# Optimization experiments

Measured on AMD Instinct MI355X. Metric: run time of the kernel, lower is better.

The kernel has to match this reference:

```python
import jax, jax.numpy as jnp
import numpy as np

N_NODES = 100000
N_EDGES = 1600000
IN_FEATS = 128
H_FEATS = 64
NEG_SLOPE = 0.2


def gat_layer(x, W, a_l, a_r, b, src, dst):
    # x: [N, Fin], W: [Fin, Fout], a_l/a_r/b: [Fout]
    h = x @ W                                   # [N, Fout]
    el = h @ a_l                                # [N]
    er = h @ a_r                                # [N]
    e = el[src] + er[dst]                       # [E]
    e = jnp.where(e > 0, e, NEG_SLOPE * e)      # leaky_relu
    # segment softmax over incoming edges of each dst node
    m = jax.ops.segment_max(e, dst, num_segments=N_NODES)   # [N], -inf for deg-0
    ex = jnp.exp(e - m[dst])                                 # [E]
    s = jax.ops.segment_sum(ex, dst, num_segments=N_NODES)   # [N]
    alpha = ex / s[dst]                                      # [E]
    out = jax.ops.segment_sum(alpha[:, None] * h[src], dst, num_segments=N_NODES)
    return jax.nn.relu(out + b)


def setup_inputs() -> dict:
    key = jax.random.key(0)
    ks = jax.random.split(key, 16)
    in_feat = jax.random.normal(ks[0], (N_NODES, IN_FEATS), dtype=jnp.float32)
    src = jax.random.randint(ks[1], (N_EDGES,), 0, N_NODES, dtype=jnp.int32)
    dst = jax.random.randint(ks[2], (N_EDGES,), 0, N_NODES, dtype=jnp.int32)
    def w(k, fin, fout):
        return jax.random.normal(k, (fin, fout), dtype=jnp.float32) * (1.0 / np.sqrt(fin))
    def v(k, f):
        return jax.random.normal(k, (f,), dtype=jnp.float32) * 0.1
    return {
        "in_feat": in_feat, "src": src, "dst": dst,
        "W1": w(ks[3], IN_FEATS, H_FEATS), "al1": v(ks[4], H_FEATS), "ar1": v(ks[5], H_FEATS), "b1": jnp.zeros((H_FEATS,), jnp.float32),
        "W2": w(ks[6], H_FEATS, H_FEATS), "al2": v(ks[7], H_FEATS), "ar2": v(ks[8], H_FEATS), "b2": jnp.zeros((H_FEATS,), jnp.float32),
        "W3": w(ks[9], H_FEATS, H_FEATS), "al3": v(ks[10], H_FEATS), "ar3": v(ks[11], H_FEATS), "b3": jnp.zeros((H_FEATS,), jnp.float32),
    }


def reference(in_feat, src, dst, W1, al1, ar1, b1, W2, al2, ar2, b2, W3, al3, ar3, b3):
    h = gat_layer(in_feat, W1, al1, ar1, b1, src, dst)
    h = gat_layer(h, W2, al2, ar2, b2, src, dst)
    h = gat_layer(h, W3, al3, ar3, b3, src, dst)
    return h
```

## Files before the change

kernel.cpp:

```cpp
#include <hip/hip_runtime.h>
#include <hip/hip_fp16.h>
#include <math.h>

#define HF 64
#define LEAKY 0.2f
#define NBLK 256
#define NPB 512
#define MAXNB 256

typedef _Float16 half4_t __attribute__((ext_vector_type(4)));
typedef _Float16 half8_t __attribute__((ext_vector_type(8)));
typedef float floatx4 __attribute__((ext_vector_type(4)));


__global__ __launch_bounds__(256)
void part_count(const int* __restrict__ dst, int* __restrict__ Cmat, int E, int nb) {
    __shared__ int lc[MAXNB];
    int tid = threadIdx.x;
    for (int t = tid; t < nb; t += 256) lc[t] = 0;
    __syncthreads();
    int chunk = (E + NBLK - 1) / NBLK;
    int b0 = blockIdx.x * chunk, b1 = min(b0 + chunk, E);
    for (int i = b0 + tid; i < b1; i += 256)
        atomicAdd(&lc[dst[i] >> 9], 1);
    __syncthreads();
    for (int t = tid; t < nb; t += 256) Cmat[t * NBLK + blockIdx.x] = lc[t];
}

__global__ __launch_bounds__(256)
void scan_offsets(const int* __restrict__ Cmat, int* __restrict__ Omat,
                  int* __restrict__ bbase, int E, int nb) {
    __shared__ int tot[256];
    int t = threadIdx.x;
    int s = 0;
    if (t < nb)
        for (int blk = 0; blk < NBLK; ++blk) s += Cmat[t * NBLK + blk];
    tot[t] = s;
    __syncthreads();
    for (int off = 1; off < 256; off <<= 1) {
        int u = (t >= off) ? tot[t - off] : 0;
        __syncthreads();
        tot[t] += u;
        __syncthreads();
    }
    int excl = tot[t] - s;
    if (t < nb) {
        bbase[t] = excl;
        int run = excl;
        for (int blk = 0; blk < NBLK; ++blk) {
            Omat[t * NBLK + blk] = run;
            run += Cmat[t * NBLK + blk];
        }
    }
    if (t == 0) bbase[nb] = E;
}

__global__ __launch_bounds__(256)
void part_scatter(const int* __restrict__ src, const int* __restrict__ dst,
                  const int* __restrict__ Omat, int2* __restrict__ part, int E, int nb) {
    __shared__ int ocur[MAXNB];
    int tid = threadIdx.x;
    for (int t = tid; t < nb; t += 256) ocur[t] = Omat[t * NBLK + blockIdx.x];
    __syncthreads();
    int chunk = (E + NBLK - 1) / NBLK;
    int b0 = blockIdx.x * chunk, b1 = min(b0 + chunk, E);
    for (int i = b0 + tid; i < b1; i += 256) {
        int s = src[i], d = dst[i];
        int pos = atomicAdd(&ocur[d >> 9], 1);
        part[pos] = make_int2(s, d);
    }
}

__global__ __launch_bounds__(NPB)
void bucket_csr(const int2* __restrict__ part, const int* __restrict__ bbase,
                int* __restrict__ row_ptr, int* __restrict__ ssrc, int N, int E, int nb) {
    int b = blockIdx.x, tid = threadIdx.x;
    int bstart = bbase[b], bend = bbase[b + 1];
    int nb0 = b << 9;
    __shared__ int cnt[NPB];
    cnt[tid] = 0;
    __syncthreads();
    for (int i = bstart + tid; i < bend; i += NPB)
        atomicAdd(&cnt[part[i].y & (NPB - 1)], 1);
    __syncthreads();
    int v = cnt[tid];
    for (int off = 1; off < NPB; off <<= 1) {
        int u = (tid >= off) ? cnt[tid - off] : 0;
        __syncthreads();
        cnt[tid] += u;
        __syncthreads();
    }
    int excl = cnt[tid] - v;
    int node = nb0 + tid;
    if (node < N) row_ptr[node] = bstart + excl;
    __syncthreads();
    cnt[tid] = bstart + excl;
    __syncthreads();
    for (int i = bstart + tid; i < bend; i += NPB) {
        int2 e = part[i];
        int slot = atomicAdd(&cnt[e.y & (NPB - 1)], 1);
        ssrc[slot] = e.x;
    }
    if (b == nb - 1 && tid == 0) row_ptr[N] = E;
}


template <int K, bool XF16>
__global__ __launch_bounds__(256, 3)
void gemm_mfma(const void* __restrict__ Xv, const float* __restrict__ W,
               const float* __restrict__ al, const float* __restrict__ ar,
               __half* __restrict__ H2, float* __restrict__ el, float* __restrict__ er,
               int n, int nslabs) {
    constexpr int KS = K / 32;
    int lane = threadIdx.x & 63;
    int li = lane & 15, g = lane >> 4;
    int wid = blockIdx.x * 4 + (threadIdx.x >> 6);
    int wstride = gridDim.x * 4;

    half8_t bf[4][KS];
    float alv[4], arv[4];
#pragma unroll
    for (int ct = 0; ct < 4; ++ct) {
        int col = ct * 16 + li;
        alv[ct] = al[col];
        arv[ct] = ar[col];
#pragma unroll
        for (int ks = 0; ks < KS; ++ks) {
            half8_t b;
#pragma unroll
            for (int j = 0; j < 4; ++j) {
                b[j]     = (_Float16)W[(ks * 32 + 4 * g + j) * 64 + col];
                b[4 + j] = (_Float16)W[(ks * 32 + 16 + 4 * g + j) * 64 + col];
            }
            bf[ct][ks] = b;
        }
    }

    for (int s = wid; s < nslabs; s += wstride) {
        int row = s * 16 + li;
        int rc = row < n ? row : n - 1;

        half8_t a[KS];
#pragma unroll
        for (int ks = 0; ks < KS; ++ks) {
            if constexpr (XF16) {
                const __half* Xh = (const __half*)Xv;
                half4_t h0 = *(const half4_t*)(Xh + (size_t)rc * K + ks * 32 + 4 * g);
                half4_t h1 = *(const half4_t*)(Xh + (size_t)rc * K + ks * 32 + 16 + 4 * g);
                half8_t av;
#pragma unroll
                for (int j = 0; j < 4; ++j) { av[j] = h0[j]; av[4 + j] = h1[j]; }
                a[ks] = av;
            } else {
                const float* Xf = (const float*)Xv;
                float4 v0 = *(const float4*)(Xf + (size_t)rc * K + ks * 32 + 4 * g);
                float4 v1 = *(const float4*)(Xf + (size_t)rc * K + ks * 32 + 16 + 4 * g);
                half8_t av;
                av[0] = (_Float16)v0.x; av[1] = (_Float16)v0.y;
                av[2] = (_Float16)v0.z; av[3] = (_Float16)v0.w;
                av[4] = (_Float16)v1.x; av[5] = (_Float16)v1.y;
                av[6] = (_Float16)v1.z; av[7] = (_Float16)v1.w;
                a[ks] = av;
            }
        }

        floatx4 acc[4];
#pragma unroll
        for (int ct = 0; ct < 4; ++ct) acc[ct] = (floatx4){0.f, 0.f, 0.f, 0.f};
#pragma unroll
        for (int ks = 0; ks < KS; ++ks)
#pragma unroll
            for (int ct = 0; ct < 4; ++ct)
                acc[ct] = __builtin_amdgcn_mfma_f32_16x16x32_f16(a[ks], bf[ct][ks], acc[ct], 0, 0, 0);

        float pl[4], pr[4];
#pragma unroll
        for (int r = 0; r < 4; ++r) {
            pl[r] = acc[0][r] * alv[0] + acc[1][r] * alv[1] + acc[2][r] * alv[2] + acc[3][r] * alv[3];
            pr[r] = acc[0][r] * arv[0] + acc[1][r] * arv[1] + acc[2][r] * arv[2] + acc[3][r] * arv[3];
        }
#pragma unroll
        for (int r = 0; r < 4; ++r)
#pragma unroll
            for (int off = 1; off < 16; off <<= 1) {
                pl[r] += __shfl_xor(pl[r], off);
                pr[r] += __shfl_xor(pr[r], off);
            }
        int rowbase = s * 16 + 4 * g;
#pragma unroll
        for (int r = 0; r < 4; ++r) {
            int ro = rowbase + r;
            if (ro < n) {
#pragma unroll
                for (int ct = 0; ct < 4; ++ct)
                    H2[(size_t)ro * HF + ct * 16 + li] = __float2half(acc[ct][r]);
                if (li == 0) { el[ro] = pl[r]; er[ro] = pr[r]; }
            }
        }
    }
}

template <bool YF16>
__device__ __forceinline__
void node_fullwave(int node, const int* __restrict__ row_ptr, const int* __restrict__ ssrc,
                   const float* __restrict__ el, const float* __restrict__ er,
                   const uint2* __restrict__ H2v, const __half* __restrict__ H2,
                   float4 bv, const float* __restrict__ b, void* __restrict__ Y,
                   int lane, int g, int fl) {
    int s0 = row_ptr[node], s1 = row_ptr[node + 1];
    int d = s1 - s0;
    float ern = er[node];

    if (d <= 64) {
        int sidx = 0;
        float e = -INFINITY;
        if (lane < d) {
            sidx = ssrc[s0 + lane];
            e = el[sidx] + ern;
            e = e > 0.f ? e : LEAKY * e;
        }
        float m = e;
#pragma unroll
        for (int off = 32; off; off >>= 1) m = fmaxf(m, __shfl_xor(m, off));
        float p = (lane < d) ? __expf(e - m) : 0.f;
        float psum = p;
#pragma unroll
        for (int off = 32; off; off >>= 1) psum += __shfl_xor(psum, off);

        float4 acc = make_float4(0.f, 0.f, 0.f, 0.f);
        int nchunk = (d + 31) >> 5;
        for (int c = 0; c < nchunk; ++c) {
            int jb = c * 32 + g;
            int ss[8];
            float pp[8];
#pragma unroll
            for (int u = 0; u < 8; ++u) {
                ss[u] = __shfl(sidx, jb + 4 * u);
                pp[u] = __shfl(p, jb + 4 * u);
            }
            uint2 vv[8];
#pragma unroll
            for (int u = 0; u < 8; ++u) vv[u] = H2v[(size_t)ss[u] * 16 + fl];
#pragma unroll
            for (int u = 0; u < 8; ++u) {
                __half2 a = *(__half2*)&vv[u].x;
                __half2 b2 = *(__half2*)&vv[u].y;
                float2 fa = __half22float2(a);
                float2 fb = __half22float2(b2);
                acc.x = fmaf(pp[u], fa.x, acc.x);
                acc.y = fmaf(pp[u], fa.y, acc.y);
                acc.z = fmaf(pp[u], fb.x, acc.z);
                acc.w = fmaf(pp[u], fb.y, acc.w);
            }
        }
#pragma unroll
        for (int off = 16; off <= 32; off <<= 1) {
            acc.x += __shfl_xor(acc.x, off);
            acc.y += __shfl_xor(acc.y, off);
            acc.z += __shfl_xor(acc.z, off);
            acc.w += __shfl_xor(acc.w, off);
        }
        float inv = d ? 1.f / psum : 0.f;
        float4 o;
        o.x = fmaf(acc.x, inv, bv.x);
        o.y = fmaf(acc.y, inv, bv.y);
        o.z = fmaf(acc.z, inv, bv.z);
        o.w = fmaf(acc.w, inv, bv.w);
        o.x = o.x > 0.f ? o.x : 0.f;
        o.y = o.y > 0.f ? o.y : 0.f;
        o.z = o.z > 0.f ? o.z : 0.f;
        o.w = o.w > 0.f ? o.w : 0.f;
        if (g == 0) {
            if constexpr (YF16) {
                __half2 a = __floats2half2_rn(o.x, o.y);
                __half2 c = __floats2half2_rn(o.z, o.w);
                ((uint2*)Y)[(size_t)node * 16 + fl] = make_uint2(*(unsigned*)&a, *(unsigned*)&c);
            } else {
                ((float4*)Y)[(size_t)node * 16 + fl] = o;
            }
        }
    } else {
        float m = -INFINITY;
        for (int j = s0 + lane; j < s1; j += 64) {
            float e = el[ssrc[j]] + ern;
            e = e > 0.f ? e : LEAKY * e;
            m = fmaxf(m, e);
        }
#pragma unroll
        for (int off = 32; off; off >>= 1) m = fmaxf(m, __shfl_xor(m, off));
        float acc = 0.f, psum = 0.f;
        for (int j = s0; j < s1; ++j) {
            int s = ssrc[j];
            float e = el[s] + ern;
            e = e > 0.f ? e : LEAKY * e;
            float p = __expf(e - m);
            psum += p;
            acc = fmaf(p, __half2float(H2[(size_t)s * HF + lane]), acc);
        }
        float o = acc / psum + b[lane];
        o = o > 0.f ? o : 0.f;
        if constexpr (YF16)
            ((__half*)Y)[(size_t)node * HF + lane] = __float2half(o);
        else
            ((float*)Y)[(size_t)node * HF + lane] = o;
    }
}

template <bool YF16>
__global__ __launch_bounds__(256)
void edge_kernel(const int* __restrict__ row_ptr, const int* __restrict__ ssrc,
                 const float* __restrict__ el, const float* __restrict__ er,
                 const __half* __restrict__ H2, const float* __restrict__ b,
                 void* __restrict__ Y, int n) {
    int wave = threadIdx.x >> 6, lane = threadIdx.x & 63;
    int half = lane >> 5, hl = lane & 31;
    int g = lane >> 4, fl = lane & 15;
    const uint2* H2v = (const uint2*)H2;
    float4 bv = ((const float4*)b)[fl];
    int npairs = (n + 1) >> 1;

    for (int pr = blockIdx.x * 4 + wave; pr < npairs; pr += gridDim.x * 4) {
        int nodeA = pr * 2;
        int myNode = nodeA + half;
        bool ok = myNode < n;
        int s0 = 0, d = 0;
        if (ok) {
            s0 = row_ptr[myNode];
            d = row_ptr[myNode + 1] - s0;
        }
        int dA = __shfl(d, 0), dB = __shfl(d, 32);

        if (dA <= 32 && dB <= 32) {
            float ern = ok ? er[myNode] : 0.f;
            int sidx = 0;
            float e = -INFINITY;
            if (hl < d) {
                sidx = ssrc[s0 + hl];
                e = el[sidx] + ern;
                e = e > 0.f ? e : LEAKY * e;
            }
            float m = e;
#pragma unroll
            for (int off = 16; off; off >>= 1) m = fmaxf(m, __shfl_xor(m, off));
            float p = (hl < d) ? __expf(e - m) : 0.f;
            float psum = p;
#pragma unroll
            for (int off = 16; off; off >>= 1) psum += __shfl_xor(psum, off);

            float4 acc = make_float4(0.f, 0.f, 0.f, 0.f);
            int dg = (g >> 1) ? dB : dA;
            int hbase = (g >> 1) << 5;
            int gpar = g & 1;
            int nch = (dg + 15) >> 4;
            for (int c = 0; c < nch; ++c) {
                int ss[8];
                float pp[8];
#pragma unroll
                for (int u = 0; u < 8; ++u) {
                    int sl = hbase + c * 16 + 2 * u + gpar;
                    ss[u] = __shfl(sidx, sl);
                    pp[u] = __shfl(p, sl);
                }
                uint2 vv[8];
#pragma unroll
                for (int u = 0; u < 8; ++u) vv[u] = H2v[(size_t)ss[u] * 16 + fl];
#pragma unroll
                for (int u = 0; u < 8; ++u) {
                    __half2 a = *(__half2*)&vv[u].x;
                    __half2 b2 = *(__half2*)&vv[u].y;
                    float2 fa = __half22float2(a);
                    float2 fb = __half22float2(b2);
                    acc.x = fmaf(pp[u], fa.x, acc.x);
                    acc.y = fmaf(pp[u], fa.y, acc.y);
                    acc.z = fmaf(pp[u], fb.x, acc.z);
                    acc.w = fmaf(pp[u], fb.y, acc.w);
                }
            }
            acc.x += __shfl_xor(acc.x, 16);
            acc.y += __shfl_xor(acc.y, 16);
            acc.z += __shfl_xor(acc.z, 16);
            acc.w += __shfl_xor(acc.w, 16);
            float inv = d ? 1.f / psum : 0.f;
            float4 o;
            o.x = fmaf(acc.x, inv, bv.x);
            o.y = fmaf(acc.y, inv, bv.y);
            o.z = fmaf(acc.z, inv, bv.z);
            o.w = fmaf(acc.w, inv, bv.w);
            o.x = o.x > 0.f ? o.x : 0.f;
            o.y = o.y > 0.f ? o.y : 0.f;
            o.z = o.z > 0.f ? o.z : 0.f;
            o.w = o.w > 0.f ? o.w : 0.f;
            if (!(g & 1) && ok) {
                if constexpr (YF16) {
                    __half2 a = __floats2half2_rn(o.x, o.y);
                    __half2 c2 = __floats2half2_rn(o.z, o.w);
                    ((uint2*)Y)[(size_t)myNode * 16 + fl] = make_uint2(*(unsigned*)&a, *(unsigned*)&c2);
                } else {
                    ((float4*)Y)[(size_t)myNode * 16 + fl] = o;
                }
            }
        } else {
            node_fullwave<YF16>(nodeA, row_ptr, ssrc, el, er, H2v, H2, bv, b, Y, lane, g, fl);
            if (nodeA + 1 < n)
                node_fullwave<YF16>(nodeA + 1, row_ptr, ssrc, el, er, H2v, H2, bv, b, Y, lane, g, fl);
        }
    }
}


extern "C" void kernel_launch(void* const* d_in, const int* in_sizes, int n_in,
                              void* d_out, int out_size, void* d_ws, size_t ws_size,
                              hipStream_t stream) {
    const int N = in_sizes[0] / 128;
    const int E = in_sizes[1];
    const int nb = (N + NPB - 1) >> 9;

    const float* in_feat = (const float*)d_in[0];
    const int* src = (const int*)d_in[1];
    const int* dst = (const int*)d_in[2];
    const float* W1 = (const float*)d_in[3];
    const float* al1 = (const float*)d_in[4];
    const float* ar1 = (const float*)d_in[5];
    const float* b1 = (const float*)d_in[6];
    const float* W2 = (const float*)d_in[7];
    const float* al2 = (const float*)d_in[8];
    const float* ar2 = (const float*)d_in[9];
    const float* b2 = (const float*)d_in[10];
    const float* W3 = (const float*)d_in[11];
    const float* al3 = (const float*)d_in[12];
    const float* ar3 = (const float*)d_in[13];
    const float* b3 = (const float*)d_in[14];

    char* ws = (char*)d_ws;
    size_t off = 0;
    auto alloc = [&](size_t bytes) {
        void* p = ws + off;
        off += (bytes + 255) & ~(size_t)255;
        return p;
    };
    int* row_ptr = (int*)alloc(((size_t)N + 1) * 4);
    int* ssrc = (int*)alloc((size_t)E * 4);
    int2* part = (int2*)alloc((size_t)E * 8);
    int* Cmat = (int*)alloc((size_t)MAXNB * NBLK * 4);
    int* Omat = (int*)alloc((size_t)MAXNB * NBLK * 4);
    int* bbase = (int*)alloc(((size_t)MAXNB + 1) * 4);
    float* el = (float*)alloc((size_t)N * 4);
    float* er = (float*)alloc((size_t)N * 4);
    __half* H2buf = (__half*)alloc((size_t)N * HF * 2);
    __half* Y2buf = (__half*)alloc((size_t)N * HF * 2);

    part_count<<<NBLK, 256, 0, stream>>>(dst, Cmat, E, nb);
    scan_offsets<<<1, 256, 0, stream>>>(Cmat, Omat, bbase, E, nb);
    part_scatter<<<NBLK, 256, 0, stream>>>(src, dst, Omat, part, E, nb);
    bucket_csr<<<nb, NPB, 0, stream>>>(part, bbase, row_ptr, ssrc, N, E, nb);

    int nslabs = (N + 15) / 16;
    int gg = 512;
    int ge = 2048;

    gemm_mfma<128, false><<<gg, 256, 0, stream>>>(in_feat, W1, al1, ar1, H2buf, el, er, N, nslabs);
    edge_kernel<true><<<ge, 256, 0, stream>>>(row_ptr, ssrc, el, er, H2buf, b1, Y2buf, N);
    gemm_mfma<64, true><<<gg, 256, 0, stream>>>(Y2buf, W2, al2, ar2, H2buf, el, er, N, nslabs);
    edge_kernel<true><<<ge, 256, 0, stream>>>(row_ptr, ssrc, el, er, H2buf, b2, Y2buf, N);
    gemm_mfma<64, true><<<gg, 256, 0, stream>>>(Y2buf, W3, al3, ar3, H2buf, el, er, N, nslabs);
    edge_kernel<false><<<ge, 256, 0, stream>>>(row_ptr, ssrc, el, er, H2buf, b3, d_out, N);
}
```

Measured before the change: 228.3 us.

## Prefetch next node pair's edges in edge kernel with contiguous per-wave ranges

The edge aggregation kernel moves from a grid-stride loop over node pairs to a contiguous block of pairs per wave. The row_ptr values for the whole block are loaded once into lanes and fetched with shuffles. The source indices, el values and er values for the next pair are prefetched while the current pair's gather and accumulation run, to hide dependent load latency. This adds register pressure, and contiguous ranges may cause load imbalance across waves.

```diff
diff --git a/kernel.cpp b/kernel.cpp
--- a/kernel.cpp
+++ b/kernel.cpp
@@ -312,40 +312,59 @@
                  const float* __restrict__ el, const float* __restrict__ er,
                  const __half* __restrict__ H2, const float* __restrict__ b,
                  void* __restrict__ Y, int n) {
-    int wave = threadIdx.x >> 6, lane = threadIdx.x & 63;
+    int lane = threadIdx.x & 63;
     int half = lane >> 5, hl = lane & 31;
     int g = lane >> 4, fl = lane & 15;
     const uint2* H2v = (const uint2*)H2;
     float4 bv = ((const float4*)b)[fl];
     int npairs = (n + 1) >> 1;
-
-    for (int pr = blockIdx.x * 4 + wave; pr < npairs; pr += gridDim.x * 4) {
-        int nodeA = pr * 2;
-        int myNode = nodeA + half;
+    int wid = blockIdx.x * 4 + (threadIdx.x >> 6);
+    int nwaves = gridDim.x * 4;
+    int PP = (npairs + nwaves - 1) / nwaves;
+    int p0 = wid * PP;
+    int p1 = min(p0 + PP, npairs);
+    if (p0 >= p1) return;
+    int cntp = p1 - p0;
+
+    int rp = 0;
+    if (lane <= 2 * cntp) rp = row_ptr[min(2 * p0 + lane, n)];
+
+    auto fetch = [&](int i, int& dd, int& sidx, float& elv, float& ernv) {
+        int myNode = 2 * (p0 + i) + half;
         bool ok = myNode < n;
-        int s0 = 0, d = 0;
-        if (ok) {
-            s0 = row_ptr[myNode];
-            d = row_ptr[myNode + 1] - s0;
-        }
-        int dA = __shfl(d, 0), dB = __shfl(d, 32);
+        int s0 = __shfl(rp, 2 * i + half);
+        int s1 = __shfl(rp, 2 * i + half + 1);
+        dd = ok ? (s1 - s0) : 0;
+        sidx = 0; elv = -INFINITY; ernv = 0.f;
+        if (ok) ernv = er[myNode];
+        if (hl < dd && dd <= 32) {
+            sidx = ssrc[s0 + hl];
+            elv = el[sidx];
+        }
+    };
+
+    int d_c, s_c; float el_c, er_c;
+    fetch(0, d_c, s_c, el_c, er_c);
+
+    for (int i = 0; i < cntp; ++i) {
+        int dA = __shfl(d_c, 0), dB = __shfl(d_c, 32);
+        bool hasnext = (i + 1 < cntp);
+        int d_n = 0, s_n = 0; float el_n = 0.f, er_n = 0.f;
+        int myNode = 2 * (p0 + i) + half;
+        bool ok = myNode < n;
 
         if (dA <= 32 && dB <= 32) {
-            float ern = ok ? er[myNode] : 0.f;
-            int sidx = 0;
-            float e = -INFINITY;
-            if (hl < d) {
-                sidx = ssrc[s0 + hl];
-                e = el[sidx] + ern;
-                e = e > 0.f ? e : LEAKY * e;
-            }
+            float e = el_c + er_c;
+            e = e > 0.f ? e : LEAKY * e;
             float m = e;
 #pragma unroll
             for (int off = 16; off; off >>= 1) m = fmaxf(m, __shfl_xor(m, off));
-            float p = (hl < d) ? __expf(e - m) : 0.f;
+            float p = (hl < d_c) ? __expf(e - m) : 0.f;
             float psum = p;
 #pragma unroll
             for (int off = 16; off; off >>= 1) psum += __shfl_xor(psum, off);
+
+            if (hasnext) fetch(i + 1, d_n, s_n, el_n, er_n);
 
             float4 acc = make_float4(0.f, 0.f, 0.f, 0.f);
             int dg = (g >> 1) ? dB : dA;
@@ -358,7 +377,7 @@
 #pragma unroll
                 for (int u = 0; u < 8; ++u) {
                     int sl = hbase + c * 16 + 2 * u + gpar;
-                    ss[u] = __shfl(sidx, sl);
+                    ss[u] = __shfl(s_c, sl);
                     pp[u] = __shfl(p, sl);
                 }
                 uint2 vv[8];
@@ -380,7 +399,7 @@
             acc.y += __shfl_xor(acc.y, 16);
             acc.z += __shfl_xor(acc.z, 16);
             acc.w += __shfl_xor(acc.w, 16);
-            float inv = d ? 1.f / psum : 0.f;
+            float inv = d_c ? 1.f / psum : 0.f;
             float4 o;
             o.x = fmaf(acc.x, inv, bv.x);
             o.y = fmaf(acc.y, inv, bv.y);
@@ -400,10 +419,14 @@
                 }
             }
         } else {
+            if (hasnext) fetch(i + 1, d_n, s_n, el_n, er_n);
+            int nodeA = 2 * (p0 + i);
             node_fullwave<YF16>(nodeA, row_ptr, ssrc, el, er, H2v, H2, bv, b, Y, lane, g, fl);
             if (nodeA + 1 < n)
                 node_fullwave<YF16>(nodeA + 1, row_ptr, ssrc, el, er, H2v, H2, bv, b, Y, lane, g, fl);
         }
+
+        d_c = d_n; s_c = s_n; el_c = el_n; er_c = er_n;
     }
 }
 
```

New measurement: 230.2 us. No clear change (+0.8%).
